# Performance work log

Hardware: AMD Instinct MI355X
Metric: run time of the kernel (lower is better)

The kernel has to match this reference:

```python
import jax, jax.numpy as jnp
import numpy as np

N = 6144          # num utterances (graph nodes)
D = 128           # utt_embed_size
WIN = 10          # att_window_size
NUM_SPK = 8
N_EMO = 7


def _init(key, shape):
    fan_in = shape[0]
    return jax.random.normal(key, shape, dtype=jnp.float32) * (1.0 / np.sqrt(fan_in))


def setup_inputs() -> dict:
    key = jax.random.key(0)
    ks = jax.random.split(key, 20)
    inp = {
        "x": jax.random.normal(ks[0], (N, D), dtype=jnp.float32),
        "speakers": jax.random.randint(ks[1], (N,), 0, NUM_SPK, dtype=jnp.int32),
        # layer-1 relation GCN weights (pred / suc / same / diff)
        "W_pred1": _init(ks[2], (D, D)),
        "W_suc1": _init(ks[3], (D, D)),
        "W_same1": _init(ks[4], (D, D)),
        "W_diff1": _init(ks[5], (D, D)),
        # layer-2 relation GCN weights
        "W_pred2": _init(ks[6], (D, D)),
        "W_suc2": _init(ks[7], (D, D)),
        "W_same2": _init(ks[8], (D, D)),
        "W_diff2": _init(ks[9], (D, D)),
        "w_aggr_1": _init(ks[10], (D, D)),
        "w_aggr_2": _init(ks[11], (D, D)),
        "w_e1": _init(ks[12], (2 * D, D)),
        "b_e1": jnp.zeros((D,), dtype=jnp.float32),
        "w_e2": _init(ks[13], (D, N_EMO)),
        "b_e2": jnp.zeros((N_EMO,), dtype=jnp.float32),
        "w_s": _init(ks[14], (2 * D, N_EMO)),
        "b_s": jnp.zeros((N_EMO,), dtype=jnp.float32),
    }
    return inp


def reference(x, speakers, W_pred1, W_suc1, W_same1, W_diff1,
              W_pred2, W_suc2, W_same2, W_diff2,
              w_aggr_1, w_aggr_2, w_e1, b_e1, w_e2, b_e2, w_s, b_s):
    n = x.shape[0]
    idx = jnp.arange(n)
    # windowed dot-product attention; entries outside the window stay 0.0
    # BEFORE the softmax (faithful to the torch code: zeros, not -inf)
    band = jnp.abs(idx[:, None] - idx[None, :]) <= WIN
    scores = jnp.where(band, x @ x.T, 0.0)            # [N, N]
    attn = jax.nn.softmax(scores, axis=1)
    # relation masks
    same = (speakers[:, None] == speakers[None, :]).astype(x.dtype)
    pred = (idx[None, :] >= idx[:, None]).astype(x.dtype)   # triu incl diag
    suc = 1.0 - pred                                          # strict lower tri
    adjs = (same * pred * attn,        # same-speaker, predecessor
            same * suc * attn,         # same-speaker, successor
            (1.0 - same) * pred * attn,  # diff-speaker, predecessor
            (1.0 - same) * suc * attn)   # diff-speaker, successor

    def gcn(h, Ws):  # sum_k adj_k @ (h @ W_k)
        return sum(a @ (h @ w) for a, w in zip(adjs, Ws))

    d = jnp.diagonal(attn)[:, None]   # self-attention scale
    h1 = jax.nn.relu(gcn(x, (W_pred1, W_suc1, W_same1, W_diff1))
                     + (x @ w_aggr_1) * d)
    h2 = jax.nn.relu(gcn(h1, (W_pred2, W_suc2, W_same2, W_diff2))
                     + (h1 @ w_aggr_2) * d)
    h = jnp.concatenate([h2, x], axis=1)              # [N, 2D]
    emotion = jax.nn.relu(h @ w_e1 + b_e1) @ w_e2 + b_e2   # [N, 7]
    sentiment = h @ w_s + b_s                               # [N, 7]
    return emotion, sentiment
```

## Files before the change

### kernel.cpp

```cpp
#include <hip/hip_runtime.h>
#include <hip/hip_bf16.h>


#define NN   6144
#define DD   128
#define WINW 10
#define YST  168
#define TAB_OFF 20544
#define SM_BYTES 26176
#define NBLK 768
#define BAR_OFF 4337664
#define BAR_STRIDE 16384
#define BAR_BYTES (3 * BAR_STRIDE)

typedef unsigned short u16;
typedef __attribute__((ext_vector_type(8))) short bf16x8;
typedef __attribute__((ext_vector_type(4))) float f32x4;

__device__ __forceinline__ float b2f(u16 u) {
    return __uint_as_float(((unsigned int)u) << 16);
}
__device__ __forceinline__ u16 f2b(float f) {
    __hip_bfloat16 h = __float2bfloat16(f);
    return *reinterpret_cast<u16*>(&h);
}
__device__ __forceinline__ bf16x8 cvt8(const float* p) {
    float4 u = *reinterpret_cast<const float4*>(p);
    float4 v = *reinterpret_cast<const float4*>(p + 4);
    bf16x8 r;
    r[0] = (short)f2b(u.x); r[1] = (short)f2b(u.y);
    r[2] = (short)f2b(u.z); r[3] = (short)f2b(u.w);
    r[4] = (short)f2b(v.x); r[5] = (short)f2b(v.y);
    r[6] = (short)f2b(v.z); r[7] = (short)f2b(v.w);
    return r;
}
__device__ __forceinline__ void st_agent_u32(unsigned* p, unsigned v) {
    __hip_atomic_store(p, v, __ATOMIC_RELAXED, __HIP_MEMORY_SCOPE_AGENT);
}
__device__ __forceinline__ void st_agent_f32(float* p, float v) {
    __hip_atomic_store(p, v, __ATOMIC_RELAXED, __HIP_MEMORY_SCOPE_AGENT);
}
__device__ __forceinline__ unsigned ld_agent_u32(const unsigned* p) {
    return __hip_atomic_load(p, __ATOMIC_RELAXED, __HIP_MEMORY_SCOPE_AGENT);
}
__device__ __forceinline__ const float* sel5(int r,
    const float* a0, const float* a1, const float* a2,
    const float* a3, const float* a4) {
    return r == 0 ? a0 : r == 1 ? a1 : r == 2 ? a2 : r == 3 ? a3 : a4;
}

__device__ __forceinline__ void grid_barrier(char* barbase, int b) {
    __syncthreads();
    if (threadIdx.x == 0) {
        char* base = barbase + b * BAR_STRIDE;
        unsigned g = blockIdx.x >> 5;
        unsigned* gctr  = (unsigned*)(base + g * 128);
        unsigned* rctr  = (unsigned*)(base + 4096);
        unsigned* gflag = (unsigned*)(base + 8192 + g * 128);
        unsigned* rflag = (unsigned*)(base + 12288);
        unsigned r = __hip_atomic_fetch_add(gctr, 1u, __ATOMIC_RELAXED,
                                            __HIP_MEMORY_SCOPE_AGENT);
        if (r == 31u) {
            unsigned rr = __hip_atomic_fetch_add(rctr, 1u, __ATOMIC_RELAXED,
                                                 __HIP_MEMORY_SCOPE_AGENT);
            if (rr == 23u) {
                st_agent_u32(rflag, 1u);
            } else {
                while (ld_agent_u32(rflag) == 0u)
                    __builtin_amdgcn_s_sleep(4);
            }
            st_agent_u32(gflag, 1u);
        } else {
            while (ld_agent_u32(gflag) == 0u)
                __builtin_amdgcn_s_sleep(4);
        }
    }
    __syncthreads();
    __builtin_amdgcn_sched_barrier(0);
}

__device__ __forceinline__ void layer_tile(
    const float* __restrict__ Af, const u16* __restrict__ Ab16,
    const u16* __restrict__ BT, const float* __restrict__ bandw,
    const int* __restrict__ spk, u16* __restrict__ hout,
    int a_is_f32, int build_tab, int hb, int bm, char* smraw, int tid)
{
    u16*  Ys  = (u16*)smraw;
    int2* tab = (int2*)(smraw + TAB_OFF);
    const int wave = tid >> 6, lane = tid & 63;
    const int lm = lane & 15, quad = lane >> 4;
    const int wm = wave >> 1, wn = wave & 1;

    if (build_tab) {
        for (int p = tid; p < 704; p += 256) {
            int il = p / 22, e = p - il * 22;
            int i  = bm + il;
            int si = spk[i];
            float w; int off;
            if (e < 21) {
                int j = i - WINW + e;
                bool valid = (j >= 0) && (j < NN);
                int jc  = valid ? j : i;
                int sel = (spk[jc] == si) ? ((j >= i) ? 0 : 1)
                                          : ((j >= i) ? 2 : 3);
                w   = valid ? bandw[(size_t)i * 32 + e] : 0.f;
                off = valid ? (il + e) * YST + sel * 32 : 0;
            } else {
                w   = bandw[(size_t)i * 32 + WINW];
                off = (il + WINW) * YST + 4 * 32;
            }
            tab[p] = make_int2(__float_as_int(w), off);
        }
    }

    bf16x8 afr[2][4];
    #pragma unroll
    for (int mt = 0; mt < 2; ++mt) {
        int gr = bm - WINW + (wm * 2 + mt) * 16 + lm;
        gr = min(max(gr, 0), NN - 1);
        #pragma unroll
        for (int s = 0; s < 4; ++s) {
            if (a_is_f32)
                afr[mt][s] = cvt8(Af + (size_t)gr * DD + s * 32 + quad * 8);
            else
                afr[mt][s] = *reinterpret_cast<const bf16x8*>(
                    Ab16 + (size_t)gr * DD + s * 32 + quad * 8);
        }
    }

    f32x4 acc[2][5];
    #pragma unroll
    for (int mt = 0; mt < 2; ++mt)
        #pragma unroll
        for (int n = 0; n < 5; ++n) acc[mt][n] = {0.f, 0.f, 0.f, 0.f};

    #pragma unroll
    for (int np = 0; np < 5; ++np) {
        int nt = wn * 5 + np;
        int gn = (nt >> 1) * 128 + hb * 32 + (nt & 1) * 16 + lm;
        #pragma unroll
        for (int s = 0; s < 4; ++s) {
            bf16x8 b = *reinterpret_cast<const bf16x8*>(
                BT + (size_t)gn * DD + s * 32 + quad * 8);
            acc[0][np] = __builtin_amdgcn_mfma_f32_16x16x32_bf16(afr[0][s], b, acc[0][np], 0, 0, 0);
            acc[1][np] = __builtin_amdgcn_mfma_f32_16x16x32_bf16(afr[1][s], b, acc[1][np], 0, 0, 0);
        }
    }
    #pragma unroll
    for (int mt = 0; mt < 2; ++mt)
        #pragma unroll
        for (int np = 0; np < 5; ++np) {
            int nt = wn * 5 + np;
            #pragma unroll
            for (int r = 0; r < 4; ++r) {
                int lr = (wm * 2 + mt) * 16 + quad * 4 + r;
                if (lr < 52) Ys[lr * YST + nt * 16 + lm] = f2b(acc[mt][np][r]);
            }
        }
    __syncthreads();

    const int c0 = (tid & 15) * 2;
    const int rg = tid >> 4;
    #pragma unroll
    for (int rr = 0; rr < 2; ++rr) {
        int il = rg * 2 + rr;
        float a0 = 0.f, a1 = 0.f;
        const int2* tp = &tab[il * 22];
        #pragma unroll
        for (int e = 0; e < 22; ++e) {
            int2 t = tp[e];
            float w = __int_as_float(t.x);
            unsigned y2 = *reinterpret_cast<const unsigned*>(Ys + t.y + c0);
            a0 = fmaf(w, b2f((u16)(y2 & 0xffff)), a0);
            a1 = fmaf(w, b2f((u16)(y2 >> 16)), a1);
        }
        int i = bm + il;
        unsigned pk = ((unsigned)f2b(fmaxf(a1, 0.f)) << 16) | f2b(fmaxf(a0, 0.f));
        st_agent_u32(reinterpret_cast<unsigned*>(
            &hout[(size_t)i * DD + hb * 32 + c0]), pk);
    }
}

__global__ __launch_bounds__(256, 4) void fused_kernel(
    const float* __restrict__ x, const int* __restrict__ spk,
    const float* __restrict__ p0, const float* __restrict__ p1,
    const float* __restrict__ p2, const float* __restrict__ p3,
    const float* __restrict__ p4,
    const float* __restrict__ q0, const float* __restrict__ q1,
    const float* __restrict__ q2, const float* __restrict__ q3,
    const float* __restrict__ q4,
    const float* __restrict__ we1, const float* __restrict__ be1,
    const float* __restrict__ we2, const float* __restrict__ be2,
    const float* __restrict__ wss, const float* __restrict__ bss,
    float* __restrict__ out, char* __restrict__ ws)
{
    float* bandw = (float*)(ws);
    u16*   W1T   = (u16*)(ws + 786432);
    u16*   W2T   = (u16*)(ws + 950272);
    u16*   We1T  = (u16*)(ws + 1114112);
    u16*   we2T  = (u16*)(ws + 1179648);
    u16*   wsT   = (u16*)(ws + 1183744);
    u16*   h1b   = (u16*)(ws + 1191936);
    u16*   h2b   = (u16*)(ws + 2764800);
    char*  bar   = ws + BAR_OFF;

    __shared__ __align__(16) char smraw[SM_BYTES];
    const int bid = blockIdx.x;
    const int tid = threadIdx.x;

    if (bid < 40) {
        int t = bid * 256 + tid;
        unsigned* W1T32 = (unsigned*)W1T;
        unsigned* W2T32 = (unsigned*)W2T;
        #pragma unroll
        for (int it = 0; it < 4; ++it) {
            int U = t + it * 10240;
            int n = U >> 6, kh = U & 63, k = kh * 2;
            int r = n >> 7, c = n & 127;
            const float* s1 = sel5(r, p0, p1, p2, p3, p4);
            const float* s2 = sel5(r, q0, q1, q2, q3, q4);
            unsigned v1 = (unsigned)f2b(s1[k * 128 + c]) |
                          ((unsigned)f2b(s1[(k + 1) * 128 + c]) << 16);
            unsigned v2 = (unsigned)f2b(s2[k * 128 + c]) |
                          ((unsigned)f2b(s2[(k + 1) * 128 + c]) << 16);
            st_agent_u32(&W1T32[U], v1);
            st_agent_u32(&W2T32[U], v2);
        }
    } else if (bid < 56) {
        int t = (bid - 40) * 256 + tid;
        unsigned* We1T32 = (unsigned*)We1T;
        #pragma unroll
        for (int it = 0; it < 4; ++it) {
            int U = t + it * 4096;
            int n = U >> 7, kh = U & 127, k = kh * 2;
            unsigned v = (unsigned)f2b(we1[k * 128 + n]) |
                         ((unsigned)f2b(we1[(k + 1) * 128 + n]) << 16);
            st_agent_u32(&We1T32[U], v);
        }
    } else if (bid == 56) {
        unsigned* we2T32 = (unsigned*)we2T;
        #pragma unroll
        for (int it = 0; it < 4; ++it) {
            int U = tid + it * 256;
            int n = U >> 6, kh = U & 63, k = kh * 2;
            float lo = n < 7 ? we2[k * 7 + n] : 0.f;
            float hi = n < 7 ? we2[(k + 1) * 7 + n] : 0.f;
            st_agent_u32(&we2T32[U],
                         (unsigned)f2b(lo) | ((unsigned)f2b(hi) << 16));
        }
    } else if (bid == 57) {
        unsigned* wsT32 = (unsigned*)wsT;
        #pragma unroll
        for (int it = 0; it < 8; ++it) {
            int U = tid + it * 256;
            int n = U >> 7, kh = U & 127, k = kh * 2;
            float lo = n < 7 ? wss[k * 7 + n] : 0.f;
            float hi = n < 7 ? wss[(k + 1) * 7 + n] : 0.f;
            st_agent_u32(&wsT32[U],
                         (unsigned)f2b(lo) | ((unsigned)f2b(hi) << 16));
        }
    } else if (bid >= 64 && bid < 448) {
        float* Xs = (float*)smraw;
        float* Ss = (float*)(smraw + 36 * 132 * 4);
        const int r0 = (bid - 64) * 16;

        #pragma unroll
        for (int it = 0; it < 5; ++it) {
            int f = tid + it * 256;
            if (f < 36 * 32) {
                int s = f >> 5, c = f & 31;
                int g = r0 - WINW + s;
                if (g >= 0 && g < NN)
                    *reinterpret_cast<float4*>(&Xs[s * 132 + c * 4]) =
                        *reinterpret_cast<const float4*>(&x[(size_t)g * DD + c * 4]);
            }
        }
        __syncthreads();

        #pragma unroll
        for (int r = 0; r < 2; ++r) {
            int p = tid + r * 256;
            if (p < 336) {
                int il = p / 21, o = p - il * 21;
                int jg = r0 + il - WINW + o;
                float sv = -1e30f;
                if (jg >= 0 && jg < NN) {
                    const float* xr = &Xs[(il + WINW) * 132];
                    const float* jr = &Xs[(il + o) * 132];
                    float a0 = 0.f, a1 = 0.f, a2 = 0.f, a3 = 0.f;
                    #pragma unroll 8
                    for (int k4 = 0; k4 < 32; ++k4) {
                        float4 a = *reinterpret_cast<const float4*>(xr + k4 * 4);
                        float4 b = *reinterpret_cast<const float4*>(jr + k4 * 4);
                        a0 = fmaf(a.x, b.x, a0); a1 = fmaf(a.y, b.y, a1);
                        a2 = fmaf(a.z, b.z, a2); a3 = fmaf(a.w, b.w, a3);
                    }
                    sv = (a0 + a1) + (a2 + a3);
                }
                Ss[il * 24 + o] = sv;
            }
        }
        __syncthreads();

        if (tid < 16) {
            int il = tid, i = r0 + il;
            float m = 0.f;
            #pragma unroll
            for (int o = 0; o < 21; ++o) {
                float s = Ss[il * 24 + o];
                if (s > -1e29f) m = fmaxf(m, s);
            }
            int lo = i - WINW; if (lo < 0) lo = 0;
            int hi = i + WINW; if (hi > NN - 1) hi = NN - 1;
            float Z = (float)(NN - (hi - lo + 1)) * expf(-m);
            float ev[21];
            #pragma unroll
            for (int o = 0; o < 21; ++o) {
                float s = Ss[il * 24 + o];
                ev[o] = (s > -1e29f) ? expf(s - m) : 0.f;
                Z += ev[o];
            }
            #pragma unroll
            for (int o = 0; o < 21; ++o)
                st_agent_f32(&bandw[i * 32 + o], ev[o] / Z);
        }
    }

    grid_barrier(bar, 0);

    {
        const int hb = bid & 3, bm = (bid >> 2) * 32;
        layer_tile(x, nullptr, W1T, bandw, spk, h1b, 1, 1, hb, bm, smraw, tid);
    }

    grid_barrier(bar, 1);

    {
        const int hb = bid & 3, bm = (bid >> 2) * 32;
        layer_tile(nullptr, h1b, W2T, bandw, spk, h2b, 0, 0, hb, bm, smraw, tid);
    }

    grid_barrier(bar, 2);

    if (bid < 384) {
        float* Es = (float*)smraw;
        const int wave = tid >> 6, lane = tid & 63;
        const int lm = lane & 15, quad = lane >> 4;
        const int bm = bid * 16;
        const int row = bm + lm;

        bf16x8 afr[8];
        #pragma unroll
        for (int s = 0; s < 4; ++s)
            afr[s] = *reinterpret_cast<const bf16x8*>(
                &h2b[(size_t)row * DD + s * 32 + quad * 8]);
        #pragma unroll
        for (int s = 4; s < 8; ++s)
            afr[s] = cvt8(&x[(size_t)row * DD + (s - 4) * 32 + quad * 8]);

        f32x4 accE[2], accS = {0.f, 0.f, 0.f, 0.f};
        #pragma unroll
        for (int n = 0; n < 2; ++n) accE[n] = {0.f, 0.f, 0.f, 0.f};

        #pragma unroll
        for (int s = 0; s < 8; ++s) {
            #pragma unroll
            for (int n = 0; n < 2; ++n) {
                int nt = wave * 2 + n;
                bf16x8 b = *reinterpret_cast<const bf16x8*>(
                    &We1T[(size_t)(nt * 16 + lm) * 256 + s * 32 + quad * 8]);
                accE[n] = __builtin_amdgcn_mfma_f32_16x16x32_bf16(afr[s], b, accE[n], 0, 0, 0);
            }
            if (wave == 0) {
                bf16x8 bsf = *reinterpret_cast<const bf16x8*>(
                    &wsT[(size_t)lm * 256 + s * 32 + quad * 8]);
                accS = __builtin_amdgcn_mfma_f32_16x16x32_bf16(afr[s], bsf, accS, 0, 0, 0);
            }
        }

        if (wave == 0 && lm < 7) {
            #pragma unroll
            for (int r = 0; r < 4; ++r) {
                int i = bm + quad * 4 + r;
                out[(size_t)NN * 7 + (size_t)i * 7 + lm] = accS[r] + bss[lm];
            }
        }
        #pragma unroll
        for (int n = 0; n < 2; ++n) {
            int col = (wave * 2 + n) * 16 + lm;
            float bias = be1[col];
            #pragma unroll
            for (int r = 0; r < 4; ++r)
                Es[(quad * 4 + r) * 132 + col] = fmaxf(accE[n][r] + bias, 0.f);
        }
        __syncthreads();

        if (wave == 0) {
            f32x4 accM = {0.f, 0.f, 0.f, 0.f};
            #pragma unroll
            for (int s = 0; s < 4; ++s) {
                bf16x8 a = cvt8(&Es[lm * 132 + s * 32 + quad * 8]);
                bf16x8 b = *reinterpret_cast<const bf16x8*>(
                    &we2T[(size_t)lm * 128 + s * 32 + quad * 8]);
                accM = __builtin_amdgcn_mfma_f32_16x16x32_bf16(a, b, accM, 0, 0, 0);
            }
            if (lm < 7) {
                #pragma unroll
                for (int r = 0; r < 4; ++r) {
                    int i = bm + quad * 4 + r;
                    out[(size_t)i * 7 + lm] = accM[r] + be2[lm];
                }
            }
        }
    }
}

extern "C" void kernel_launch(void* const* d_in, const int* in_sizes, int n_in,
                              void* d_out, int out_size, void* d_ws, size_t ws_size,
                              hipStream_t stream)
{
    const float* x   = (const float*)d_in[0];
    const int*   spk = (const int*)d_in[1];
    const float* Wp1 = (const float*)d_in[2];
    const float* Wu1 = (const float*)d_in[3];
    const float* Wm1 = (const float*)d_in[4];
    const float* Wd1 = (const float*)d_in[5];
    const float* Wp2 = (const float*)d_in[6];
    const float* Wu2 = (const float*)d_in[7];
    const float* Wm2 = (const float*)d_in[8];
    const float* Wd2 = (const float*)d_in[9];
    const float* wa1 = (const float*)d_in[10];
    const float* wa2 = (const float*)d_in[11];
    const float* we1 = (const float*)d_in[12];
    const float* be1 = (const float*)d_in[13];
    const float* we2 = (const float*)d_in[14];
    const float* be2 = (const float*)d_in[15];
    const float* wss = (const float*)d_in[16];
    const float* bss = (const float*)d_in[17];
    float* out = (float*)d_out;
    char*  ws  = (char*)d_ws;

    hipMemsetAsync(ws + BAR_OFF, 0, BAR_BYTES, stream);

    fused_kernel<<<dim3(NBLK), dim3(256), 0, stream>>>(
        x, spk, Wp1, Wu1, Wm1, Wd1, wa1, Wp2, Wu2, Wm2, Wd2, wa2,
        we1, be1, we2, be2, wss, bss, out, ws);
}
```

Measured before the change: 139.6 us.

## Fuse band-softmax into layer-1 tile, drop global attention buffer

Band attention scores and softmax weights are now computed inside each layer-1 tile from an LDS-staged x window, so the global bandw buffer and its phase-0 producer blocks disappear. The weight transpose prologue is spread over more blocks with coalesced source reads. Block-to-tile mapping changes from interleaved column blocks to hb-major, the head phase gets a swizzled row order, and barrier spin sleep is shortened. The cost is that each of the four column blocks sharing a row tile recomputes the same softmax, and LDS use per block grows.

```diff
diff --git a/kernel.cpp b/kernel.cpp
--- a/kernel.cpp
+++ b/kernel.cpp
@@ -6,10 +6,18 @@
 #define DD   128
 #define WINW 10
 #define YST  168
-#define TAB_OFF 20544
-#define SM_BYTES 26176
+#define TAB_OFF 27456
+#define SS_OFF  33088
+#define SM_BYTES 35904
 #define NBLK 768
-#define BAR_OFF 4337664
+#define WS_W1T 0
+#define WS_W2T 163840
+#define WS_WE1 327680
+#define WS_WE2 393216
+#define WS_WST 397312
+#define WS_H1  405504
+#define WS_H2  1978368
+#define BAR_OFF 3551232
 #define BAR_STRIDE 16384
 #define BAR_BYTES (3 * BAR_STRIDE)
 
@@ -35,9 +43,6 @@
     return r;
 }
 __device__ __forceinline__ void st_agent_u32(unsigned* p, unsigned v) {
-    __hip_atomic_store(p, v, __ATOMIC_RELAXED, __HIP_MEMORY_SCOPE_AGENT);
-}
-__device__ __forceinline__ void st_agent_f32(float* p, float v) {
     __hip_atomic_store(p, v, __ATOMIC_RELAXED, __HIP_MEMORY_SCOPE_AGENT);
 }
 __device__ __forceinline__ unsigned ld_agent_u32(const unsigned* p) {
@@ -67,12 +72,12 @@
                 st_agent_u32(rflag, 1u);
             } else {
                 while (ld_agent_u32(rflag) == 0u)
-                    __builtin_amdgcn_s_sleep(4);
+                    __builtin_amdgcn_s_sleep(1);
             }
             st_agent_u32(gflag, 1u);
         } else {
             while (ld_agent_u32(gflag) == 0u)
-                __builtin_amdgcn_s_sleep(4);
+                __builtin_amdgcn_s_sleep(1);
         }
     }
     __syncthreads();
@@ -80,209 +85,40 @@
 }
 
 __device__ __forceinline__ void layer_tile(
-    const float* __restrict__ Af, const u16* __restrict__ Ab16,
-    const u16* __restrict__ BT, const float* __restrict__ bandw,
-    const int* __restrict__ spk, u16* __restrict__ hout,
-    int a_is_f32, int build_tab, int hb, int bm, char* smraw, int tid)
+    const float* __restrict__ x, const u16* __restrict__ Ab16,
+    const u16* __restrict__ BT, const int* __restrict__ spk,
+    u16* __restrict__ hout, int first_layer, int hb, int bm,
+    char* smraw, int tid)
 {
-    u16*  Ys  = (u16*)smraw;
-    int2* tab = (int2*)(smraw + TAB_OFF);
+    u16*   Ys  = (u16*)smraw;
+    float* Xs  = (float*)smraw;
+    int2*  tab = (int2*)(smraw + TAB_OFF);
+    float* Ss  = (float*)(smraw + SS_OFF);
     const int wave = tid >> 6, lane = tid & 63;
     const int lm = lane & 15, quad = lane >> 4;
     const int wm = wave >> 1, wn = wave & 1;
 
-    if (build_tab) {
-        for (int p = tid; p < 704; p += 256) {
-            int il = p / 22, e = p - il * 22;
-            int i  = bm + il;
-            int si = spk[i];
-            float w; int off;
-            if (e < 21) {
-                int j = i - WINW + e;
-                bool valid = (j >= 0) && (j < NN);
-                int jc  = valid ? j : i;
-                int sel = (spk[jc] == si) ? ((j >= i) ? 0 : 1)
-                                          : ((j >= i) ? 2 : 3);
-                w   = valid ? bandw[(size_t)i * 32 + e] : 0.f;
-                off = valid ? (il + e) * YST + sel * 32 : 0;
-            } else {
-                w   = bandw[(size_t)i * 32 + WINW];
-                off = (il + WINW) * YST + 4 * 32;
-            }
-            tab[p] = make_int2(__float_as_int(w), off);
-        }
-    }
-
     bf16x8 afr[2][4];
-    #pragma unroll
-    for (int mt = 0; mt < 2; ++mt) {
-        int gr = bm - WINW + (wm * 2 + mt) * 16 + lm;
-        gr = min(max(gr, 0), NN - 1);
-        #pragma unroll
-        for (int s = 0; s < 4; ++s) {
-            if (a_is_f32)
-                afr[mt][s] = cvt8(Af + (size_t)gr * DD + s * 32 + quad * 8);
-            else
-                afr[mt][s] = *reinterpret_cast<const bf16x8*>(
-                    Ab16 + (size_t)gr * DD + s * 32 + quad * 8);
-        }
-    }
-
-    f32x4 acc[2][5];
-    #pragma unroll
-    for (int mt = 0; mt < 2; ++mt)
-        #pragma unroll
-        for (int n = 0; n < 5; ++n) acc[mt][n] = {0.f, 0.f, 0.f, 0.f};
-
-    #pragma unroll
-    for (int np = 0; np < 5; ++np) {
-        int nt = wn * 5 + np;
-        int gn = (nt >> 1) * 128 + hb * 32 + (nt & 1) * 16 + lm;
-        #pragma unroll
-        for (int s = 0; s < 4; ++s) {
-            bf16x8 b = *reinterpret_cast<const bf16x8*>(
-                BT + (size_t)gn * DD + s * 32 + quad * 8);
-            acc[0][np] = __builtin_amdgcn_mfma_f32_16x16x32_bf16(afr[0][s], b, acc[0][np], 0, 0, 0);
-            acc[1][np] = __builtin_amdgcn_mfma_f32_16x16x32_bf16(afr[1][s], b, acc[1][np], 0, 0, 0);
-        }
-    }
-    #pragma unroll
-    for (int mt = 0; mt < 2; ++mt)
-        #pragma unroll
-        for (int np = 0; np < 5; ++np) {
-            int nt = wn * 5 + np;
-            #pragma unroll
-            for (int r = 0; r < 4; ++r) {
-                int lr = (wm * 2 + mt) * 16 + quad * 4 + r;
-                if (lr < 52) Ys[lr * YST + nt * 16 + lm] = f2b(acc[mt][np][r]);
-            }
-        }
-    __syncthreads();
-
-    const int c0 = (tid & 15) * 2;
-    const int rg = tid >> 4;
-    #pragma unroll
-    for (int rr = 0; rr < 2; ++rr) {
-        int il = rg * 2 + rr;
-        float a0 = 0.f, a1 = 0.f;
-        const int2* tp = &tab[il * 22];
-        #pragma unroll
-        for (int e = 0; e < 22; ++e) {
-            int2 t = tp[e];
-            float w = __int_as_float(t.x);
-            unsigned y2 = *reinterpret_cast<const unsigned*>(Ys + t.y + c0);
-            a0 = fmaf(w, b2f((u16)(y2 & 0xffff)), a0);
-            a1 = fmaf(w, b2f((u16)(y2 >> 16)), a1);
-        }
-        int i = bm + il;
-        unsigned pk = ((unsigned)f2b(fmaxf(a1, 0.f)) << 16) | f2b(fmaxf(a0, 0.f));
-        st_agent_u32(reinterpret_cast<unsigned*>(
-            &hout[(size_t)i * DD + hb * 32 + c0]), pk);
-    }
-}
-
-__global__ __launch_bounds__(256, 4) void fused_kernel(
-    const float* __restrict__ x, const int* __restrict__ spk,
-    const float* __restrict__ p0, const float* __restrict__ p1,
-    const float* __restrict__ p2, const float* __restrict__ p3,
-    const float* __restrict__ p4,
-    const float* __restrict__ q0, const float* __restrict__ q1,
-    const float* __restrict__ q2, const float* __restrict__ q3,
-    const float* __restrict__ q4,
-    const float* __restrict__ we1, const float* __restrict__ be1,
-    const float* __restrict__ we2, const float* __restrict__ be2,
-    const float* __restrict__ wss, const float* __restrict__ bss,
-    float* __restrict__ out, char* __restrict__ ws)
-{
-    float* bandw = (float*)(ws);
-    u16*   W1T   = (u16*)(ws + 786432);
-    u16*   W2T   = (u16*)(ws + 950272);
-    u16*   We1T  = (u16*)(ws + 1114112);
-    u16*   we2T  = (u16*)(ws + 1179648);
-    u16*   wsT   = (u16*)(ws + 1183744);
-    u16*   h1b   = (u16*)(ws + 1191936);
-    u16*   h2b   = (u16*)(ws + 2764800);
-    char*  bar   = ws + BAR_OFF;
-
-    __shared__ __align__(16) char smraw[SM_BYTES];
-    const int bid = blockIdx.x;
-    const int tid = threadIdx.x;
-
-    if (bid < 40) {
-        int t = bid * 256 + tid;
-        unsigned* W1T32 = (unsigned*)W1T;
-        unsigned* W2T32 = (unsigned*)W2T;
-        #pragma unroll
-        for (int it = 0; it < 4; ++it) {
-            int U = t + it * 10240;
-            int n = U >> 6, kh = U & 63, k = kh * 2;
-            int r = n >> 7, c = n & 127;
-            const float* s1 = sel5(r, p0, p1, p2, p3, p4);
-            const float* s2 = sel5(r, q0, q1, q2, q3, q4);
-            unsigned v1 = (unsigned)f2b(s1[k * 128 + c]) |
-                          ((unsigned)f2b(s1[(k + 1) * 128 + c]) << 16);
-            unsigned v2 = (unsigned)f2b(s2[k * 128 + c]) |
-                          ((unsigned)f2b(s2[(k + 1) * 128 + c]) << 16);
-            st_agent_u32(&W1T32[U], v1);
-            st_agent_u32(&W2T32[U], v2);
-        }
-    } else if (bid < 56) {
-        int t = (bid - 40) * 256 + tid;
-        unsigned* We1T32 = (unsigned*)We1T;
-        #pragma unroll
-        for (int it = 0; it < 4; ++it) {
-            int U = t + it * 4096;
-            int n = U >> 7, kh = U & 127, k = kh * 2;
-            unsigned v = (unsigned)f2b(we1[k * 128 + n]) |
-                         ((unsigned)f2b(we1[(k + 1) * 128 + n]) << 16);
-            st_agent_u32(&We1T32[U], v);
-        }
-    } else if (bid == 56) {
-        unsigned* we2T32 = (unsigned*)we2T;
-        #pragma unroll
-        for (int it = 0; it < 4; ++it) {
-            int U = tid + it * 256;
-            int n = U >> 6, kh = U & 63, k = kh * 2;
-            float lo = n < 7 ? we2[k * 7 + n] : 0.f;
-            float hi = n < 7 ? we2[(k + 1) * 7 + n] : 0.f;
-            st_agent_u32(&we2T32[U],
-                         (unsigned)f2b(lo) | ((unsigned)f2b(hi) << 16));
-        }
-    } else if (bid == 57) {
-        unsigned* wsT32 = (unsigned*)wsT;
-        #pragma unroll
-        for (int it = 0; it < 8; ++it) {
-            int U = tid + it * 256;
-            int n = U >> 7, kh = U & 127, k = kh * 2;
-            float lo = n < 7 ? wss[k * 7 + n] : 0.f;
-            float hi = n < 7 ? wss[(k + 1) * 7 + n] : 0.f;
-            st_agent_u32(&wsT32[U],
-                         (unsigned)f2b(lo) | ((unsigned)f2b(hi) << 16));
-        }
-    } else if (bid >= 64 && bid < 448) {
-        float* Xs = (float*)smraw;
-        float* Ss = (float*)(smraw + 36 * 132 * 4);
-        const int r0 = (bid - 64) * 16;
-
-        #pragma unroll
-        for (int it = 0; it < 5; ++it) {
+
+    if (first_layer) {
+        #pragma unroll
+        for (int it = 0; it < 7; ++it) {
             int f = tid + it * 256;
-            if (f < 36 * 32) {
+            if (f < 52 * 32) {
                 int s = f >> 5, c = f & 31;
-                int g = r0 - WINW + s;
-                if (g >= 0 && g < NN)
-                    *reinterpret_cast<float4*>(&Xs[s * 132 + c * 4]) =
-                        *reinterpret_cast<const float4*>(&x[(size_t)g * DD + c * 4]);
+                int g = min(max(bm - WINW + s, 0), NN - 1);
+                *reinterpret_cast<float4*>(&Xs[s * 132 + c * 4]) =
+                    *reinterpret_cast<const float4*>(&x[(size_t)g * DD + c * 4]);
             }
         }
         __syncthreads();
 
         #pragma unroll
-        for (int r = 0; r < 2; ++r) {
-            int p = tid + r * 256;
-            if (p < 336) {
+        for (int rr = 0; rr < 3; ++rr) {
+            int p = tid + rr * 256;
+            if (p < 672) {
                 int il = p / 21, o = p - il * 21;
-                int jg = r0 + il - WINW + o;
+                int jg = bm + il - WINW + o;
                 float sv = -1e30f;
                 if (jg >= 0 && jg < NN) {
                     const float* xr = &Xs[(il + WINW) * 132];
@@ -297,48 +133,215 @@
                     }
                     sv = (a0 + a1) + (a2 + a3);
                 }
-                Ss[il * 24 + o] = sv;
+                Ss[il * 22 + o] = sv;
             }
         }
         __syncthreads();
 
-        if (tid < 16) {
-            int il = tid, i = r0 + il;
+        if (tid < 32) {
+            int il = tid, i = bm + il;
             float m = 0.f;
             #pragma unroll
             for (int o = 0; o < 21; ++o) {
-                float s = Ss[il * 24 + o];
+                float s = Ss[il * 22 + o];
                 if (s > -1e29f) m = fmaxf(m, s);
             }
             int lo = i - WINW; if (lo < 0) lo = 0;
             int hi = i + WINW; if (hi > NN - 1) hi = NN - 1;
-            float Z = (float)(NN - (hi - lo + 1)) * expf(-m);
+            float Z = (float)(NN - (hi - lo + 1)) * __expf(-m);
             float ev[21];
             #pragma unroll
             for (int o = 0; o < 21; ++o) {
-                float s = Ss[il * 24 + o];
-                ev[o] = (s > -1e29f) ? expf(s - m) : 0.f;
+                float s = Ss[il * 22 + o];
+                ev[o] = (s > -1e29f) ? __expf(s - m) : 0.f;
                 Z += ev[o];
             }
-            #pragma unroll
-            for (int o = 0; o < 21; ++o)
-                st_agent_f32(&bandw[i * 32 + o], ev[o] / Z);
+            float rz = 1.f / Z;
+            #pragma unroll
+            for (int o = 0; o < 21; ++o) Ss[il * 22 + o] = ev[o] * rz;
+        }
+        __syncthreads();
+
+        #pragma unroll
+        for (int rr = 0; rr < 3; ++rr) {
+            int p = tid + rr * 256;
+            if (p < 704) {
+                int il = p / 22, e = p - il * 22;
+                int i  = bm + il;
+                int si = spk[i];
+                float w; int off;
+                if (e < 21) {
+                    int j = i - WINW + e;
+                    bool valid = (j >= 0) && (j < NN);
+                    int jc  = valid ? j : i;
+                    int sel = (spk[jc] == si) ? ((j >= i) ? 0 : 1)
+                                              : ((j >= i) ? 2 : 3);
+                    w   = valid ? Ss[il * 22 + e] : 0.f;
+                    off = valid ? (il + e) * YST + sel * 32 : 0;
+                } else {
+                    w   = Ss[il * 22 + WINW];
+                    off = (il + WINW) * YST + 4 * 32;
+                }
+                tab[p] = make_int2(__float_as_int(w), off);
+            }
+        }
+
+        #pragma unroll
+        for (int mt = 0; mt < 2; ++mt) {
+            int rl = min((wm * 2 + mt) * 16 + lm, 51);
+            #pragma unroll
+            for (int s = 0; s < 4; ++s)
+                afr[mt][s] = cvt8(&Xs[rl * 132 + s * 32 + quad * 8]);
+        }
+        __syncthreads();
+    } else {
+        #pragma unroll
+        for (int mt = 0; mt < 2; ++mt) {
+            int gr = min(max(bm - WINW + (wm * 2 + mt) * 16 + lm, 0), NN - 1);
+            #pragma unroll
+            for (int s = 0; s < 4; ++s)
+                afr[mt][s] = *reinterpret_cast<const bf16x8*>(
+                    Ab16 + (size_t)gr * DD + s * 32 + quad * 8);
+        }
+    }
+
+    f32x4 acc[2][5];
+    #pragma unroll
+    for (int mt = 0; mt < 2; ++mt)
+        #pragma unroll
+        for (int n = 0; n < 5; ++n) acc[mt][n] = {0.f, 0.f, 0.f, 0.f};
+
+    #pragma unroll
+    for (int np = 0; np < 5; ++np) {
+        int nt = wn * 5 + np;
+        int gn = (nt >> 1) * 128 + hb * 32 + (nt & 1) * 16 + lm;
+        #pragma unroll
+        for (int s = 0; s < 4; ++s) {
+            bf16x8 b = *reinterpret_cast<const bf16x8*>(
+                BT + (size_t)gn * DD + s * 32 + quad * 8);
+            acc[0][np] = __builtin_amdgcn_mfma_f32_16x16x32_bf16(afr[0][s], b, acc[0][np], 0, 0, 0);
+            acc[1][np] = __builtin_amdgcn_mfma_f32_16x16x32_bf16(afr[1][s], b, acc[1][np], 0, 0, 0);
+        }
+    }
+    #pragma unroll
+    for (int mt = 0; mt < 2; ++mt)
+        #pragma unroll
+        for (int np = 0; np < 5; ++np) {
+            int nt = wn * 5 + np;
+            #pragma unroll
+            for (int r = 0; r < 4; ++r) {
+                int lr = (wm * 2 + mt) * 16 + quad * 4 + r;
+                if (lr < 52) Ys[lr * YST + nt * 16 + lm] = f2b(acc[mt][np][r]);
+            }
+        }
+    __syncthreads();
+
+    const int c0 = (tid & 15) * 2;
+    const int rg = tid >> 4;
+    #pragma unroll
+    for (int rr = 0; rr < 2; ++rr) {
+        int il = rg * 2 + rr;
+        float a0 = 0.f, a1 = 0.f;
+        const int2* tp = &tab[il * 22];
+        #pragma unroll
+        for (int e = 0; e < 22; ++e) {
+            int2 t = tp[e];
+            float w = __int_as_float(t.x);
+            unsigned y2 = *reinterpret_cast<const unsigned*>(Ys + t.y + c0);
+            a0 = fmaf(w, b2f((u16)(y2 & 0xffff)), a0);
+            a1 = fmaf(w, b2f((u16)(y2 >> 16)), a1);
+        }
+        int i = bm + il;
+        unsigned pk = ((unsigned)f2b(fmaxf(a1, 0.f)) << 16) | f2b(fmaxf(a0, 0.f));
+        st_agent_u32(reinterpret_cast<unsigned*>(
+            &hout[(size_t)i * DD + hb * 32 + c0]), pk);
+    }
+}
+
+__global__ __launch_bounds__(256, 4) void fused_kernel(
+    const float* __restrict__ x, const int* __restrict__ spk,
+    const float* __restrict__ p0, const float* __restrict__ p1,
+    const float* __restrict__ p2, const float* __restrict__ p3,
+    const float* __restrict__ p4,
+    const float* __restrict__ q0, const float* __restrict__ q1,
+    const float* __restrict__ q2, const float* __restrict__ q3,
+    const float* __restrict__ q4,
+    const float* __restrict__ we1, const float* __restrict__ be1,
+    const float* __restrict__ we2, const float* __restrict__ be2,
+    const float* __restrict__ wss, const float* __restrict__ bss,
+    float* __restrict__ out, char* __restrict__ ws)
+{
+    u16*   W1T   = (u16*)(ws + WS_W1T);
+    u16*   W2T   = (u16*)(ws + WS_W2T);
+    u16*   We1T  = (u16*)(ws + WS_WE1);
+    u16*   we2T  = (u16*)(ws + WS_WE2);
+    u16*   wsT   = (u16*)(ws + WS_WST);
+    u16*   h1b   = (u16*)(ws + WS_H1);
+    u16*   h2b   = (u16*)(ws + WS_H2);
+    char*  bar   = ws + BAR_OFF;
+
+    __shared__ __align__(16) char smraw[SM_BYTES];
+    const int bid = blockIdx.x;
+    const int tid = threadIdx.x;
+
+    if (bid < 160) {
+        unsigned* W1T32 = (unsigned*)W1T;
+        unsigned* W2T32 = (unsigned*)W2T;
+        int idx = bid * 256 + tid;
+        int c = idx & 127, rk = idx >> 7;
+        int r = rk >> 6, k2 = rk & 63, k = k2 * 2;
+        const float* s1 = sel5(r, p0, p1, p2, p3, p4);
+        const float* s2 = sel5(r, q0, q1, q2, q3, q4);
+        unsigned v1 = (unsigned)f2b(s1[k * 128 + c]) |
+                      ((unsigned)f2b(s1[(k + 1) * 128 + c]) << 16);
+        unsigned v2 = (unsigned)f2b(s2[k * 128 + c]) |
+                      ((unsigned)f2b(s2[(k + 1) * 128 + c]) << 16);
+        int U = (r * 128 + c) * 64 + k2;
+        st_agent_u32(&W1T32[U], v1);
+        st_agent_u32(&W2T32[U], v2);
+    } else if (bid < 192) {
+        unsigned* We1T32 = (unsigned*)We1T;
+        #pragma unroll
+        for (int it = 0; it < 2; ++it) {
+            int idx = (bid - 160) * 256 + tid + it * 8192;
+            int n = idx & 127, k2 = idx >> 7, k = k2 * 2;
+            unsigned v = (unsigned)f2b(we1[k * 128 + n]) |
+                         ((unsigned)f2b(we1[(k + 1) * 128 + n]) << 16);
+            st_agent_u32(&We1T32[n * 128 + k2], v);
+        }
+    } else if (bid == 192) {
+        unsigned* we2T32 = (unsigned*)we2T;
+        #pragma unroll
+        for (int it = 0; it < 4; ++it) {
+            int U = tid + it * 256;
+            int n = U >> 6, kh = U & 63, k = kh * 2;
+            float lo = n < 7 ? we2[k * 7 + n] : 0.f;
+            float hi = n < 7 ? we2[(k + 1) * 7 + n] : 0.f;
+            st_agent_u32(&we2T32[U],
+                         (unsigned)f2b(lo) | ((unsigned)f2b(hi) << 16));
+        }
+    } else if (bid == 193) {
+        unsigned* wsT32 = (unsigned*)wsT;
+        #pragma unroll
+        for (int it = 0; it < 8; ++it) {
+            int U = tid + it * 256;
+            int n = U >> 7, kh = U & 127, k = kh * 2;
+            float lo = n < 7 ? wss[k * 7 + n] : 0.f;
+            float hi = n < 7 ? wss[(k + 1) * 7 + n] : 0.f;
+            st_agent_u32(&wsT32[U],
+                         (unsigned)f2b(lo) | ((unsigned)f2b(hi) << 16));
         }
     }
 
     grid_barrier(bar, 0);
 
-    {
-        const int hb = bid & 3, bm = (bid >> 2) * 32;
-        layer_tile(x, nullptr, W1T, bandw, spk, h1b, 1, 1, hb, bm, smraw, tid);
-    }
+    const int hb = bid / 192, bmi = bid - hb * 192;
+    const int bm = bmi * 32;
+    layer_tile(x, nullptr, W1T, spk, h1b, 1, hb, bm, smraw, tid);
 
     grid_barrier(bar, 1);
 
-    {
-        const int hb = bid & 3, bm = (bid >> 2) * 32;
-        layer_tile(nullptr, h1b, W2T, bandw, spk, h2b, 0, 0, hb, bm, smraw, tid);
-    }
+    layer_tile(nullptr, h1b, W2T, spk, h2b, 0, hb, bm, smraw, tid);
 
     grid_barrier(bar, 2);
 
@@ -346,8 +349,9 @@
         float* Es = (float*)smraw;
         const int wave = tid >> 6, lane = tid & 63;
         const int lm = lane & 15, quad = lane >> 4;
-        const int bm = bid * 16;
-        const int row = bm + lm;
+        const int rt = (bid & ~15) | ((bid & 7) << 1) | ((bid >> 3) & 1);
+        const int bmh = rt * 16;
+        const int row = bmh + lm;
 
         bf16x8 afr[8];
         #pragma unroll
@@ -381,7 +385,7 @@
         if (wave == 0 && lm < 7) {
             #pragma unroll
             for (int r = 0; r < 4; ++r) {
-                int i = bm + quad * 4 + r;
+                int i = bmh + quad * 4 + r;
                 out[(size_t)NN * 7 + (size_t)i * 7 + lm] = accS[r] + bss[lm];
             }
         }
@@ -407,7 +411,7 @@
             if (lm < 7) {
                 #pragma unroll
                 for (int r = 0; r < 4; ++r) {
-                    int i = bm + quad * 4 + r;
+                    int i = bmh + quad * 4 + r;
                     out[(size_t)i * 7 + lm] = accM[r] + be2[lm];
                 }
             }
```

New measurement: 137.7 us. About the same (-1.4%).
